# Performance work log

Measured on AMD Instinct MI355X. Metric: run time of the kernel, lower is better.

Reference implementation:

```python
import jax, jax.numpy as jnp
import numpy as np

B, S, L = 2, 1024, 1024
DIM_Q, H, K, D_C, D_CQ, R = 2048, 16, 128, 512, 1536, 64


def _rope_tables(length, dim):
    # matches _RoPECache._build_tables: repeat_interleave(2) layout
    inv = 1.0 / (10000.0 ** (jnp.arange(0, dim, 2, dtype=jnp.float32) / dim))
    f = jnp.arange(length, dtype=jnp.float32)[:, None] * inv[None, :]  # [len, dim/2]
    sin = jnp.repeat(jnp.sin(f), 2, axis=-1)
    cos = jnp.repeat(jnp.cos(f), 2, axis=-1)
    return sin, cos


def _rotate_half(x):
    half = x.shape[-1] // 2
    return jnp.concatenate([-x[..., half:], x[..., :half]], axis=-1)


def _apply_rope(x, sin, cos):
    return x * cos + _rotate_half(x) * sin


def setup_inputs() -> dict:
    key = jax.random.key(0)
    ks = jax.random.split(key, 8)
    return {
        "hidden_q": jax.random.normal(ks[0], (B, S, DIM_Q), jnp.float32),
        "kv_c": jax.random.normal(ks[1], (B, L, D_C), jnp.float32),
        "Wq": jax.random.normal(ks[2], (H * K, DIM_Q), jnp.float32) / np.sqrt(DIM_Q).astype(np.float32),
        "w_kc_q": jax.random.normal(ks[3], (H, K, D_CQ), jnp.float32) / np.sqrt(K).astype(np.float32),
        "w_kc_kv": jax.random.normal(ks[4], (H, K, D_C), jnp.float32) / np.sqrt(K).astype(np.float32),
        "W_qr": jax.random.normal(ks[5], (H, D_CQ, R), jnp.float32) / np.float32(np.sqrt(D_CQ) * np.sqrt(R)),
        "W_kr": jax.random.normal(ks[6], (H, D_C, R), jnp.float32) / np.sqrt(D_C).astype(np.float32),
        "Wo": jax.random.normal(ks[7], (DIM_Q, H * K), jnp.float32) / np.sqrt(H * K).astype(np.float32),
    }


def reference(hidden_q, kv_c, Wq, w_kc_q, w_kc_kv, W_qr, W_kr, Wo):
    Bv, Sv, _ = hidden_q.shape
    _, Lv, _ = kv_c.shape
    # latent -> per-head queries, then decompress to d_cq
    q_hk = (hidden_q @ Wq.T).reshape(Bv, Sv, H, K)          # [B,S,H,K]
    q_big = jnp.einsum('bshk,hkq->bshq', q_hk, w_kc_q)      # [B,S,H,d_cq]
    sin_q, cos_q = _rope_tables(Sv, D_CQ)
    q_big = _apply_rope(q_big, sin_q[None, :, None, :], cos_q[None, :, None, :])
    sin_k, cos_k = _rope_tables(Lv, D_C)
    kv_r = _apply_rope(kv_c, sin_k[None], cos_k[None])      # [B,L,d_c]
    # retrieval projections (scale 1/sqrt(r) baked into W_qr)
    q_r = jnp.einsum('bshq,hqr->bhsr', q_big, W_qr)         # [B,H,S,r]
    k_r = jnp.einsum('bld,hdr->bhlr', kv_r, W_kr)           # [B,H,L,r]
    scores = jnp.einsum('bhsr,bhlr->bhsl', q_r, k_r)
    attn = jax.nn.softmax(scores, axis=-1)
    # values are the (RoPE'd) compressed kv shared across heads
    ctx_c = jnp.einsum('bhsl,bld->bhsd', attn, kv_r)        # [B,H,S,d_c]
    # decompress context: w_kc_kv.transpose(1,2) is [H,d_c,K]
    ctx_lat = jnp.einsum('bhsd,hkd->bhsk', ctx_c, w_kc_kv)  # [B,H,S,K]
    ctx = ctx_lat.transpose(0, 2, 1, 3).reshape(Bv, Sv, H * K)
    return ctx @ Wo.T
```

## Files before the change

### kernel.cpp

```cpp
#include <hip/hip_runtime.h>
#include <hip/hip_bf16.h>


typedef __attribute__((ext_vector_type(8))) short short8;
typedef __attribute__((ext_vector_type(4))) float f32x4;

__device__ __forceinline__ unsigned short f2bs(float v){
  __hip_bfloat16 b = __float2bfloat16(v);
  return *reinterpret_cast<unsigned short*>(&b);
}
__device__ __forceinline__ void storeC(float* p, float v){ *p = v; }
__device__ __forceinline__ void storeC(unsigned short* p, float v){ *p = f2bs(v); }

__device__ __forceinline__ void gl_lds16(const void* g, void* l){
  __builtin_amdgcn_global_load_lds(
      (const __attribute__((address_space(1))) unsigned int*)g,
      (__attribute__((address_space(3))) unsigned int*)l, 16, 0, 0);
}

template<int N> __device__ __forceinline__ void wait_vmcnt(){
  if constexpr (N==0)       asm volatile("s_waitcnt vmcnt(0)" ::: "memory");
  else if constexpr (N==3)  asm volatile("s_waitcnt vmcnt(3)" ::: "memory");
  else if constexpr (N==4)  asm volatile("s_waitcnt vmcnt(4)" ::: "memory");
  else if constexpr (N==6)  asm volatile("s_waitcnt vmcnt(6)" ::: "memory");
  else if constexpr (N==8)  asm volatile("s_waitcnt vmcnt(8)" ::: "memory");
  else if constexpr (N==14) asm volatile("s_waitcnt vmcnt(14)" ::: "memory");
  else if constexpr (N==16) asm volatile("s_waitcnt vmcnt(16)" ::: "memory");
  else if constexpr (N==22) asm volatile("s_waitcnt vmcnt(22)" ::: "memory");
  else static_assert(N==0, "unsupported vmcnt");
}

__global__ __launch_bounds__(256) void prep_all(
    float4* __restrict__ rq,
    float* __restrict__ sink, float* __restrict__ cosk,
    const float* __restrict__ hidden, unsigned short* __restrict__ hiddenb,
    const float* __restrict__ Wq, unsigned short* __restrict__ Wqb,
    const float* __restrict__ wkckv, unsigned short* __restrict__ wkckvb,
    const float* __restrict__ Wo, unsigned short* __restrict__ Wob)
{
  int blk = blockIdx.x;
  if (blk < 3072){
    int idx = blk*256 + threadIdx.x;
    int s = idx / 768, j = idx - (idx/768)*768;
    int i1 = j >> 1;
    const float cst = -0.011992631f;
    float f1 = (float)s * __expf(cst * (float)i1);
    float f2 = (float)s * __expf(cst * (float)(384 + i1));
    float s1, c1, s2, c2;
    __sincosf(f1, &s1, &c1);
    __sincosf(f2, &s2, &c2);
    rq[idx] = make_float4(c1, s1, c2, s2);
    return;
  }
  if (blk < 4096){
    int idx = (blk-3072)*256 + threadIdx.x;
    int l = idx >> 8, j = idx & 255;
    const float cst = -0.035977892f;
    float f = (float)l * __expf(cst * (float)j);
    float sv, cv; __sincosf(f, &sv, &cv);
    int base = l*512 + 2*j;
    sink[base] = sv; sink[base+1] = sv;
    cosk[base] = cv; cosk[base+1] = cv;
    return;
  }
  const float* in; unsigned short* out; int i;
  if (blk < 8192){ in = hidden; out = hiddenb; i = (blk-4096)*256 + threadIdx.x; }
  else if (blk < 12288){ in = Wq; out = Wqb; i = (blk-8192)*256 + threadIdx.x; }
  else if (blk < 13312){ in = wkckv; out = wkckvb; i = (blk-12288)*256 + threadIdx.x; }
  else { in = Wo; out = Wob; i = (blk-13312)*256 + threadIdx.x; }
  float4 v = *(const float4*)(in + (long)i*4);
  ushort4 u; u.x=f2bs(v.x); u.y=f2bs(v.y); u.z=f2bs(v.z); u.w=f2bs(v.w);
  *(ushort4*)(out + (long)i*4) = u;
}

__global__ __launch_bounds__(256) void transpose_cvt(
    const float* __restrict__ in, unsigned short* __restrict__ out,
    int R, int Cn, long sIn, long sOut)
{
  __shared__ float tile[32][33];
  const float* ip = in + (long)blockIdx.z*sIn;
  unsigned short* op = out + (long)blockIdx.z*sOut;
  int c0 = blockIdx.x*32, r0 = blockIdx.y*32;
  int tr = threadIdx.x>>5, tc = threadIdx.x&31;
  #pragma unroll
  for (int i=0;i<4;i++)
    tile[tr+i*8][tc] = ip[(long)(r0+tr+i*8)*Cn + c0+tc];
  __syncthreads();
  #pragma unroll
  for (int i=0;i<4;i++)
    op[(long)(c0+tr+i*8)*R + r0+tc] = f2bs(tile[tc][tr+i*8]);
}

template<int BM,int BN,int WM,int WN,typename TC>
__global__ __launch_bounds__(256) void gemm_mfma(
    const unsigned short* __restrict__ A, const unsigned short* __restrict__ B,
    TC* __restrict__ C,
    int Kd, int lda, int ldb, int ldc, int Hb,
    long sAb, long sAh, long sBb, long sBh, long sCb, long sCh)
{
  constexpr int MF = WM/16, NF = WN/16;
  constexpr int WGM = BM/WM;
  constexpr int AOPS = (4*BM)/256;
  constexpr int BOPS = (4*BN)/256;
  constexpr int STG  = AOPS + BOPS;

  const int z = blockIdx.z, bb = z/Hb, hh = z - bb*Hb;
  const unsigned short* Ap = A + bb*sAb + hh*sAh;
  const unsigned short* Bp = B + bb*sBb + hh*sBh;
  TC* Cp = C + bb*sCb + hh*sCh;
  const int m0 = blockIdx.x*BM, n0 = blockIdx.y*BN;
  const int t = threadIdx.x, w = t>>6, l = t&63;
  const int wm0 = (w % WGM)*WM, wn0 = (w / WGM)*WN;
  const int lq = l>>4, lm = l&15;

  __shared__ __align__(16) unsigned short As[4][4*BM*8];
  __shared__ __align__(16) unsigned short Bs[4][4*BN*8];

  f32x4 acc[MF][NF];
  #pragma unroll
  for (int mf=0; mf<MF; ++mf)
    #pragma unroll
    for (int nf=0; nf<NF; ++nf)
      acc[mf][nf] = f32x4{0.f,0.f,0.f,0.f};

  auto stage = [&](int buf, int k0){
    #pragma unroll
    for (int o = 0; o < AOPS; ++o){
      int g = o*256 + t;
      int row = g & (BM-1), kq = g / BM;
      gl_lds16(Ap + (long)(m0+row)*lda + k0 + kq*8, &As[buf][(o*256 + w*64)*8]);
    }
    #pragma unroll
    for (int o = 0; o < BOPS; ++o){
      int g = o*256 + t;
      int row = g & (BN-1), kq = g / BN;
      gl_lds16(Bp + (long)(n0+row)*ldb + k0 + kq*8, &Bs[buf][(o*256 + w*64)*8]);
    }
  };

  const int nIter = Kd >> 5;
  stage(0, 0);
  if (1 < nIter) stage(1, 32);
  if (2 < nIter) stage(2, 64);

  for (int it = 0; it < nIter; ++it){
    const int cur = it & 3;
    const int rem = nIter - it;
    if (rem >= 3)      wait_vmcnt<2*STG>();
    else if (rem == 2) wait_vmcnt<STG>();
    else               wait_vmcnt<0>();
    __builtin_amdgcn_s_barrier();

    short8 af[MF], bfr[NF];
    #pragma unroll
    for (int mf=0; mf<MF; ++mf)
      af[mf] = *(const short8*)&As[cur][(lq*BM + wm0 + mf*16 + lm)*8];
    #pragma unroll
    for (int nf=0; nf<NF; ++nf)
      bfr[nf] = *(const short8*)&Bs[cur][(lq*BN + wn0 + nf*16 + lm)*8];
    #pragma unroll
    for (int mf=0; mf<MF; ++mf)
      #pragma unroll
      for (int nf=0; nf<NF; ++nf)
        acc[mf][nf] = __builtin_amdgcn_mfma_f32_16x16x32_bf16(
            af[mf], bfr[nf], acc[mf][nf], 0, 0, 0);

    if (it+3 < nIter) stage((it+3) & 3, (it+3)*32);
  }

  #pragma unroll
  for (int mf=0; mf<MF; ++mf){
    #pragma unroll
    for (int nf=0; nf<NF; ++nf){
      int row = m0 + wm0 + mf*16 + lq*4;
      int col = n0 + wn0 + nf*16 + lm;
      #pragma unroll
      for (int r=0; r<4; ++r)
        storeC(&Cp[(long)(row+r)*ldc + col], acc[mf][nf][r]);
    }
  }
}

__global__ __launch_bounds__(256) void q_fused(
    const unsigned short* __restrict__ A,
    const unsigned short* __restrict__ W1t,
    const unsigned short* __restrict__ W2t,
    const float4* __restrict__ rq,
    unsigned short* __restrict__ qrOut)
{
  const int z = blockIdx.z, bb = z>>4, hh = z&15;
  const int m0 = blockIdx.x*64;
  const unsigned short* Ap = A + (long)bb*2097152 + hh*128;
  const unsigned short* W1 = W1t + (long)hh*196608;
  const unsigned short* W2 = W2t + (long)hh*98304;
  unsigned short* qo = qrOut + ((long)z*1024 + m0)*64;

  const int t = threadIdx.x, w = t>>6, l = t&63;
  const int lq = l>>4, lm = l&15;

  __shared__ __align__(16) unsigned short As[16*64*8];
  __shared__ __align__(16) unsigned short W1s[2][16*64*8];
  __shared__ __align__(16) unsigned short W2s[2][8*64*8];
  __shared__ __align__(16) unsigned short Ps[64*72];

  #pragma unroll
  for (int o=0;o<4;++o){
    int g=o*256+t; int row=g&63, kq=g>>6;
    gl_lds16(Ap + (long)(m0+row)*2048 + kq*8, &As[(o*256+w*64)*8]);
  }
  auto stageW = [&](int buf, int cn){
    #pragma unroll
    for (int o=0;o<4;++o){
      int g=o*256+t; int row=g&63, kq=g>>6;
      int grow = (row<32) ? (cn*32+row) : (736+cn*32+row);
      gl_lds16(W1 + (long)grow*128 + kq*8, &W1s[buf][(o*256+w*64)*8]);
    }
    #pragma unroll
    for (int o=0;o<2;++o){
      int g=o*256+t; int n=g&63, kq=g>>6;
      int qk = (kq<4) ? (cn*32+kq*8) : (736+cn*32+kq*8);
      gl_lds16(W2 + (long)n*1536 + qk, &W2s[buf][(o*256+w*64)*8]);
    }
  };
  stageW(0, 0);
  __syncthreads();

  short8 af[4];
  #pragma unroll
  for (int ks=0; ks<4; ++ks)
    af[ks] = *(const short8*)&As[((ks*4+lq)*64 + w*16 + lm)*8];

  f32x4 accr[4];
  #pragma unroll
  for (int nf=0; nf<4; ++nf) accr[nf] = f32x4{0.f,0.f,0.f,0.f};

  for (int cn = 0; cn < 24; ++cn){
    const int cur = cn & 1;

    float4 rc_reg[2][4];
    #pragma unroll
    for (int nf=0; nf<2; ++nf)
      #pragma unroll
      for (int r=0; r<4; ++r){
        int srow = m0 + w*16 + lq*4 + r;
        rc_reg[nf][r] = rq[(long)srow*768 + cn*32 + nf*16 + lm];
      }
    if (cn < 23) stageW(cur^1, cn+1);
    if (cn < 23) wait_vmcnt<14>(); else wait_vmcnt<8>();
    __builtin_amdgcn_s_barrier();

    f32x4 sa[4];
    #pragma unroll
    for (int nf=0; nf<4; ++nf) sa[nf] = f32x4{0.f,0.f,0.f,0.f};
    #pragma unroll
    for (int ks=0; ks<4; ++ks)
      #pragma unroll
      for (int nf=0; nf<4; ++nf){
        short8 bf = *(const short8*)&W1s[cur][((ks*4+lq)*64 + nf*16 + lm)*8];
        sa[nf] = __builtin_amdgcn_mfma_f32_16x16x32_bf16(af[ks], bf, sa[nf], 0,0,0);
      }

    #pragma unroll
    for (int nf=0; nf<2; ++nf)
      #pragma unroll
      for (int r=0; r<4; ++r){
        int prow = w*16 + lq*4 + r;
        float4 rc = rc_reg[nf][r];
        float xl = sa[nf][r], xh = sa[nf+2][r];
        Ps[prow*72 + nf*16 + lm]      = f2bs(xl*rc.x - xh*rc.y);
        Ps[prow*72 + 32 + nf*16 + lm] = f2bs(xh*rc.z + xl*rc.w);
      }

    #pragma unroll
    for (int ks=0; ks<2; ++ks){
      short8 ap = *(const short8*)&Ps[(w*16 + lm)*72 + ks*32 + lq*8];
      #pragma unroll
      for (int nf=0; nf<4; ++nf){
        short8 bw = *(const short8*)&W2s[cur][((ks*4+lq)*64 + nf*16 + lm)*8];
        accr[nf] = __builtin_amdgcn_mfma_f32_16x16x32_bf16(ap, bw, accr[nf], 0,0,0);
      }
    }
    __builtin_amdgcn_s_barrier();
  }

  #pragma unroll
  for (int nf=0; nf<4; ++nf)
    #pragma unroll
    for (int r=0; r<4; ++r)
      qo[(long)(w*16 + lq*4 + r)*64 + nf*16 + lm] = f2bs(accr[nf][r]);
}

__global__ __launch_bounds__(256) void rope_k_kernel(
    const float* __restrict__ kc,
    const float* __restrict__ sk, const float* __restrict__ ck,
    unsigned short* __restrict__ kvrb)
{
  int idx = blockIdx.x*256 + threadIdx.x;
  int row = idx >> 8;
  int d = idx & 255;
  int l = row & 1023;
  long base = (long)row*512;
  float xl = kc[base+d], xh = kc[base+d+256];
  int tb = l*512 + d;
  kvrb[base+d]     = f2bs(xl*ck[tb]     - xh*sk[tb]);
  kvrb[base+d+256] = f2bs(xh*ck[tb+256] + xl*sk[tb+256]);
}

__global__ __launch_bounds__(256) void flash_mfma(
    const unsigned short* __restrict__ qr, const unsigned short* __restrict__ kr,
    const unsigned short* __restrict__ vt, unsigned short* __restrict__ ctx)
{
  const int b = blockIdx.z, h = blockIdx.y, s0 = blockIdx.x*64;
  const int t = threadIdx.x, w = t>>6, l = t&63;
  const int lq = l>>4, lm = l&15;

  __shared__ __align__(16) unsigned short Qs[8*64*8];
  __shared__ __align__(16) unsigned short Ks[2][8*64*8];
  __shared__ __align__(16) unsigned short Vts[2][8*128*8];
  __shared__ __align__(16) unsigned short Ps[64*72];

  const unsigned short* qbase = qr + ((long)(b*16+h)*1024 + s0)*64;
  const unsigned short* kbase = kr + (long)(b*16+h)*65536;
  const unsigned short* vbase = vt + (long)(b*16+h)*131072;

  auto stageKV = [&](int buf, int l0){
    #pragma unroll
    for (int o = 0; o < 2; ++o){
      int g = o*256 + t;
      int row = g & 63, kq = g >> 6;
      gl_lds16(kbase + (long)(l0+row)*64 + kq*8, &Ks[buf][(o*256 + w*64)*8]);
    }
    #pragma unroll
    for (int o = 0; o < 4; ++o){
      int g = o*256 + t;
      int row = g & 127, kq = g >> 7;
      gl_lds16(vbase + (long)row*1024 + l0 + kq*8, &Vts[buf][(o*256 + w*64)*8]);
    }
  };

  #pragma unroll
  for (int o = 0; o < 2; ++o){
    int g = o*256 + t;
    int row = g & 63, kq = g >> 6;
    gl_lds16(qbase + (long)row*64 + kq*8, &Qs[(o*256 + w*64)*8]);
  }
  stageKV(0, 0);
  __syncthreads();
  short8 aq[2];
  #pragma unroll
  for (int ks = 0; ks < 2; ++ks)
    aq[ks] = *(const short8*)&Qs[((ks*4+lq)*64 + w*16 + lm)*8];

  float m_run[4], l_run[4];
  #pragma unroll
  for (int r = 0; r < 4; ++r){ m_run[r] = -3e38f; l_run[r] = 0.f; }
  f32x4 acc_o[8];
  #pragma unroll
  for (int nf = 0; nf < 8; ++nf) acc_o[nf] = f32x4{0.f,0.f,0.f,0.f};

  for (int it = 0; it < 16; ++it){
    const int cur = it & 1;
    if (it < 15){ stageKV(cur^1, (it+1)*64); wait_vmcnt<6>(); }
    else        { wait_vmcnt<0>(); }
    __builtin_amdgcn_s_barrier();

    f32x4 acc_s[4];
    #pragma unroll
    for (int nf = 0; nf < 4; ++nf) acc_s[nf] = f32x4{0.f,0.f,0.f,0.f};
    #pragma unroll
    for (int ks = 0; ks < 2; ++ks)
      #pragma unroll
      for (int nf = 0; nf < 4; ++nf){
        short8 bf = *(const short8*)&Ks[cur][((ks*4+lq)*64 + nf*16 + lm)*8];
        acc_s[nf] = __builtin_amdgcn_mfma_f32_16x16x32_bf16(
            aq[ks], bf, acc_s[nf], 0, 0, 0);
      }

    float tmax[4];
    #pragma unroll
    for (int r = 0; r < 4; ++r)
      tmax[r] = fmaxf(fmaxf(acc_s[0][r], acc_s[1][r]),
                      fmaxf(acc_s[2][r], acc_s[3][r]));
    #pragma unroll
    for (int mask = 1; mask < 16; mask <<= 1)
      #pragma unroll
      for (int r = 0; r < 4; ++r)
        tmax[r] = fmaxf(tmax[r], __shfl_xor(tmax[r], mask));
    float alpha[4], rsum[4];
    #pragma unroll
    for (int r = 0; r < 4; ++r){
      float mnew = fmaxf(m_run[r], tmax[r]);
      alpha[r] = __expf(m_run[r] - mnew);
      m_run[r] = mnew;
      rsum[r] = 0.f;
    }
    #pragma unroll
    for (int nf = 0; nf < 4; ++nf)
      #pragma unroll
      for (int r = 0; r < 4; ++r){
        float p = __expf(acc_s[nf][r] - m_run[r]);
        rsum[r] += p;
        Ps[(w*16 + lq*4 + r)*72 + nf*16 + lm] = f2bs(p);
      }
    #pragma unroll
    for (int mask = 1; mask < 16; mask <<= 1)
      #pragma unroll
      for (int r = 0; r < 4; ++r)
        rsum[r] += __shfl_xor(rsum[r], mask);
    #pragma unroll
    for (int r = 0; r < 4; ++r)
      l_run[r] = l_run[r]*alpha[r] + rsum[r];

    #pragma unroll
    for (int nf = 0; nf < 8; ++nf)
      #pragma unroll
      for (int r = 0; r < 4; ++r)
        acc_o[nf][r] *= alpha[r];

    short8 ap[2];
    #pragma unroll
    for (int ks = 0; ks < 2; ++ks)
      ap[ks] = *(const short8*)&Ps[(w*16 + lm)*72 + ks*32 + lq*8];
    #pragma unroll
    for (int ks = 0; ks < 2; ++ks)
      #pragma unroll
      for (int nf = 0; nf < 8; ++nf){
        short8 bv = *(const short8*)&Vts[cur][((ks*4+lq)*128 + nf*16 + lm)*8];
        acc_o[nf] = __builtin_amdgcn_mfma_f32_16x16x32_bf16(
            ap[ks], bv, acc_o[nf], 0, 0, 0);
      }
    __builtin_amdgcn_s_barrier();
  }

  float inv[4];
  #pragma unroll
  for (int r = 0; r < 4; ++r) inv[r] = 1.f / l_run[r];
  #pragma unroll
  for (int nf = 0; nf < 8; ++nf)
    #pragma unroll
    for (int r = 0; r < 4; ++r){
      long row = (long)b*1024 + s0 + w*16 + lq*4 + r;
      ctx[row*2048 + h*128 + nf*16 + lm] = f2bs(acc_o[nf][r]*inv[r]);
    }
}

extern "C" void kernel_launch(void* const* d_in, const int* in_sizes, int n_in,
                              void* d_out, int out_size, void* d_ws, size_t ws_size,
                              hipStream_t stream)
{
  const float* hidden_q = (const float*)d_in[0];
  const float* kv_c     = (const float*)d_in[1];
  const float* Wq       = (const float*)d_in[2];
  const float* w_kc_q   = (const float*)d_in[3];
  const float* w_kc_kv  = (const float*)d_in[4];
  const float* W_qr     = (const float*)d_in[5];
  const float* W_kr     = (const float*)d_in[6];
  const float* Wo       = (const float*)d_in[7];
  float* out = (float*)d_out;

  char* wsb = (char*)d_ws;
  size_t off = 0;
  auto take = [&](size_t bytes)->void*{
    void* p = wsb + off; off += (bytes + 255) & ~(size_t)255; return p;
  };
  unsigned short* q_rb  = (unsigned short*)take(4194304);
  unsigned short* k_rb  = (unsigned short*)take(4194304);
  unsigned short* kv_rb = (unsigned short*)take(2097152);
  float* sink   = (float*)take(2097152);
  float* cosk   = (float*)take(2097152);
  float4* ropeq4 = (float4*)take(12582912);
  unsigned short* q_hk   = (unsigned short*)take(8388608);
  unsigned short* wkcqT  = (unsigned short*)take(6291456);
  unsigned short* WqrT   = (unsigned short*)take(3145728);
  unsigned short* wkckvb = (unsigned short*)take(2097152);
  unsigned short* WkrT   = (unsigned short*)take(1048576);
  unsigned short* Vt     = (unsigned short*)take(8388608);
  unsigned short* hiddenb = (unsigned short*)take(8388608);
  unsigned short* Wqb     = (unsigned short*)take(8388608);
  unsigned short* Wob     = (unsigned short*)take(8388608);
  unsigned short* ctx_lat = (unsigned short*)take(8388608);

  prep_all<<<17408, 256, 0, stream>>>(ropeq4, sink, cosk,
      hidden_q, hiddenb, Wq, Wqb, w_kc_kv, wkckvb, Wo, Wob);
  transpose_cvt<<<dim3(48,4,16), 256, 0, stream>>>(w_kc_q, wkcqT, 128, 1536, 196608, 196608);
  transpose_cvt<<<dim3(2,48,16), 256, 0, stream>>>(W_qr, WqrT, 1536, 64, 98304, 98304);
  transpose_cvt<<<dim3(2,16,16), 256, 0, stream>>>(W_kr, WkrT, 512, 64, 32768, 32768);

  gemm_mfma<128,128,64,64,unsigned short><<<dim3(16,16,1),256,0,stream>>>(
      hiddenb, Wqb, q_hk, 2048, 2048,2048,2048, 1, 0,0, 0,0, 0,0);

  q_fused<<<dim3(16,1,32),256,0,stream>>>(q_hk, wkcqT, WqrT, ropeq4, q_rb);

  rope_k_kernel<<<2048, 256, 0, stream>>>(kv_c, sink, cosk, kv_rb);

  gemm_mfma<128,64,64,32,unsigned short><<<dim3(8,1,32),256,0,stream>>>(
      kv_rb, WkrT, k_rb, 512, 512,512,64, 16,
      524288,0, 0,32768, 1048576,65536);

  gemm_mfma<128,128,64,64,unsigned short><<<dim3(1,8,32),256,0,stream>>>(
      wkckvb, kv_rb, Vt, 512, 512,512,1024, 16,
      0,65536, 524288,0, 2097152,131072);

  flash_mfma<<<dim3(16,16,2),256,0,stream>>>(q_rb, k_rb, Vt, ctx_lat);

  gemm_mfma<128,128,64,64,float><<<dim3(16,16,1),256,0,stream>>>(
      ctx_lat, Wob, out, 2048, 2048,2048,2048, 1, 0,0, 0,0, 0,0);
}
```

Measured before the change: 343.5 us.

## Fuse prep kernels, compute K rope inline, and retile q_fused warps

Merges the three transpose_cvt launches and the rope_k kernel into the single prep_all launch. The K-side RoPE now computes sin/cos on the fly and writes rotated bf16 kv directly, which drops the sin/cos tables and their global round trip. q_fused changes its warp layout to 2x2 (32 rows by half the columns per warp), loads A fragments straight from global instead of through LDS, and adds an extra barrier before reading Ps. The aims are fewer launches, less memory traffic and better B-fragment reuse, at the cost of an extra sync per chunk in q_fused.

```diff
diff --git a/kernel.cpp b/kernel.cpp
--- a/kernel.cpp
+++ b/kernel.cpp
@@ -30,13 +30,30 @@
   else static_assert(N==0, "unsupported vmcnt");
 }
 
+__device__ __forceinline__ void transpose_tile(
+    const float* ip, unsigned short* op, int R, int Cn, int c0, int r0)
+{
+  __shared__ float tile[32][33];
+  int tr = threadIdx.x>>5, tc = threadIdx.x&31;
+  #pragma unroll
+  for (int i=0;i<4;i++)
+    tile[tr+i*8][tc] = ip[(long)(r0+tr+i*8)*Cn + c0+tc];
+  __syncthreads();
+  #pragma unroll
+  for (int i=0;i<4;i++)
+    op[(long)(c0+tr+i*8)*R + r0+tc] = f2bs(tile[tc][tr+i*8]);
+}
+
 __global__ __launch_bounds__(256) void prep_all(
     float4* __restrict__ rq,
-    float* __restrict__ sink, float* __restrict__ cosk,
+    const float* __restrict__ kvc, unsigned short* __restrict__ kvrb,
     const float* __restrict__ hidden, unsigned short* __restrict__ hiddenb,
     const float* __restrict__ Wq, unsigned short* __restrict__ Wqb,
     const float* __restrict__ wkckv, unsigned short* __restrict__ wkckvb,
-    const float* __restrict__ Wo, unsigned short* __restrict__ Wob)
+    const float* __restrict__ Wo, unsigned short* __restrict__ Wob,
+    const float* __restrict__ wkcq, unsigned short* __restrict__ wkcqT,
+    const float* __restrict__ Wqr, unsigned short* __restrict__ WqrT,
+    const float* __restrict__ Wkr, unsigned short* __restrict__ WkrT)
 {
   int blk = blockIdx.x;
   if (blk < 3072){
@@ -54,41 +71,55 @@
   }
   if (blk < 4096){
     int idx = (blk-3072)*256 + threadIdx.x;
-    int l = idx >> 8, j = idx & 255;
+    int i1 = idx & 127;
+    int l  = (idx >> 7) & 1023;
+    int bb = idx >> 17;
     const float cst = -0.035977892f;
-    float f = (float)l * __expf(cst * (float)j);
-    float sv, cv; __sincosf(f, &sv, &cv);
-    int base = l*512 + 2*j;
-    sink[base] = sv; sink[base+1] = sv;
-    cosk[base] = cv; cosk[base+1] = cv;
+    float f1 = (float)l * __expf(cst * (float)i1);
+    float f2 = (float)l * __expf(cst * (float)(128 + i1));
+    float s1,c1,s2,c2; __sincosf(f1,&s1,&c1); __sincosf(f2,&s2,&c2);
+    long base = ((long)bb*1024 + l)*512;
+    float2 xlo = *(const float2*)&kvc[base + 2*i1];
+    float2 xhi = *(const float2*)&kvc[base + 2*i1 + 256];
+    unsigned int lo = (unsigned)f2bs(xlo.x*c1 - xhi.x*s1)
+                    | ((unsigned)f2bs(xlo.y*c1 - xhi.y*s1) << 16);
+    unsigned int hi = (unsigned)f2bs(xhi.x*c2 + xlo.x*s2)
+                    | ((unsigned)f2bs(xhi.y*c2 + xlo.y*s2) << 16);
+    *(unsigned int*)&kvrb[base + 2*i1]       = lo;
+    *(unsigned int*)&kvrb[base + 2*i1 + 256] = hi;
     return;
   }
-  const float* in; unsigned short* out; int i;
-  if (blk < 8192){ in = hidden; out = hiddenb; i = (blk-4096)*256 + threadIdx.x; }
-  else if (blk < 12288){ in = Wq; out = Wqb; i = (blk-8192)*256 + threadIdx.x; }
-  else if (blk < 13312){ in = wkckv; out = wkckvb; i = (blk-12288)*256 + threadIdx.x; }
-  else { in = Wo; out = Wob; i = (blk-13312)*256 + threadIdx.x; }
-  float4 v = *(const float4*)(in + (long)i*4);
-  ushort4 u; u.x=f2bs(v.x); u.y=f2bs(v.y); u.z=f2bs(v.z); u.w=f2bs(v.w);
-  *(ushort4*)(out + (long)i*4) = u;
-}
-
-__global__ __launch_bounds__(256) void transpose_cvt(
-    const float* __restrict__ in, unsigned short* __restrict__ out,
-    int R, int Cn, long sIn, long sOut)
-{
-  __shared__ float tile[32][33];
-  const float* ip = in + (long)blockIdx.z*sIn;
-  unsigned short* op = out + (long)blockIdx.z*sOut;
-  int c0 = blockIdx.x*32, r0 = blockIdx.y*32;
-  int tr = threadIdx.x>>5, tc = threadIdx.x&31;
-  #pragma unroll
-  for (int i=0;i<4;i++)
-    tile[tr+i*8][tc] = ip[(long)(r0+tr+i*8)*Cn + c0+tc];
-  __syncthreads();
-  #pragma unroll
-  for (int i=0;i<4;i++)
-    op[(long)(c0+tr+i*8)*R + r0+tc] = f2bs(tile[tc][tr+i*8]);
+  if (blk < 17408){
+    const float* in; unsigned short* out; int i;
+    if (blk < 8192){ in = hidden; out = hiddenb; i = (blk-4096)*256 + threadIdx.x; }
+    else if (blk < 12288){ in = Wq; out = Wqb; i = (blk-8192)*256 + threadIdx.x; }
+    else if (blk < 13312){ in = wkckv; out = wkckvb; i = (blk-12288)*256 + threadIdx.x; }
+    else { in = Wo; out = Wob; i = (blk-13312)*256 + threadIdx.x; }
+    float4 v = *(const float4*)(in + (long)i*4);
+    ushort4 u; u.x=f2bs(v.x); u.y=f2bs(v.y); u.z=f2bs(v.z); u.w=f2bs(v.w);
+    *(ushort4*)(out + (long)i*4) = u;
+    return;
+  }
+  if (blk < 20480){
+    int b2 = blk - 17408;
+    int x = b2 % 48, rem = b2 / 48, y = rem % 4, z = rem >> 2;
+    transpose_tile(wkcq + (long)z*196608, wkcqT + (long)z*196608,
+                   128, 1536, x*32, y*32);
+    return;
+  }
+  if (blk < 22016){
+    int b2 = blk - 20480;
+    int x = b2 & 1, rem = b2 >> 1, y = rem % 48, z = rem / 48;
+    transpose_tile(Wqr + (long)z*98304, WqrT + (long)z*98304,
+                   1536, 64, x*32, y*32);
+    return;
+  }
+  {
+    int b2 = blk - 22016;
+    int x = b2 & 1, y = (b2 >> 1) & 15, z = b2 >> 5;
+    transpose_tile(Wkr + (long)z*32768, WkrT + (long)z*32768,
+                   512, 64, x*32, y*32);
+  }
 }
 
 template<int BM,int BN,int WM,int WN,typename TC>
@@ -197,17 +228,20 @@
 
   const int t = threadIdx.x, w = t>>6, l = t&63;
   const int lq = l>>4, lm = l&15;
-
-  __shared__ __align__(16) unsigned short As[16*64*8];
+  const int wr = (w>>1)*32;
+  const int wc = w&1;
+
   __shared__ __align__(16) unsigned short W1s[2][16*64*8];
   __shared__ __align__(16) unsigned short W2s[2][8*64*8];
   __shared__ __align__(16) unsigned short Ps[64*72];
 
-  #pragma unroll
-  for (int o=0;o<4;++o){
-    int g=o*256+t; int row=g&63, kq=g>>6;
-    gl_lds16(Ap + (long)(m0+row)*2048 + kq*8, &As[(o*256+w*64)*8]);
-  }
+  short8 af[2][4];
+  #pragma unroll
+  for (int mf=0; mf<2; ++mf)
+    #pragma unroll
+    for (int ks=0; ks<4; ++ks)
+      af[mf][ks] = *(const short8*)&Ap[(long)(m0 + wr + mf*16 + lm)*2048 + (ks*4+lq)*8];
+
   auto stageW = [&](int buf, int cn){
     #pragma unroll
     for (int o=0;o<4;++o){
@@ -223,87 +257,78 @@
     }
   };
   stageW(0, 0);
-  __syncthreads();
-
-  short8 af[4];
-  #pragma unroll
-  for (int ks=0; ks<4; ++ks)
-    af[ks] = *(const short8*)&As[((ks*4+lq)*64 + w*16 + lm)*8];
-
-  f32x4 accr[4];
-  #pragma unroll
-  for (int nf=0; nf<4; ++nf) accr[nf] = f32x4{0.f,0.f,0.f,0.f};
+
+  f32x4 accr[2][2];
+  #pragma unroll
+  for (int mf=0; mf<2; ++mf)
+    #pragma unroll
+    for (int nf=0; nf<2; ++nf) accr[mf][nf] = f32x4{0.f,0.f,0.f,0.f};
 
   for (int cn = 0; cn < 24; ++cn){
     const int cur = cn & 1;
 
     float4 rc_reg[2][4];
     #pragma unroll
-    for (int nf=0; nf<2; ++nf)
+    for (int mf=0; mf<2; ++mf)
       #pragma unroll
       for (int r=0; r<4; ++r){
-        int srow = m0 + w*16 + lq*4 + r;
-        rc_reg[nf][r] = rq[(long)srow*768 + cn*32 + nf*16 + lm];
+        int srow = m0 + wr + mf*16 + lq*4 + r;
+        rc_reg[mf][r] = rq[(long)srow*768 + cn*32 + wc*16 + lm];
       }
     if (cn < 23) stageW(cur^1, cn+1);
     if (cn < 23) wait_vmcnt<14>(); else wait_vmcnt<8>();
     __builtin_amdgcn_s_barrier();
 
-    f32x4 sa[4];
-    #pragma unroll
-    for (int nf=0; nf<4; ++nf) sa[nf] = f32x4{0.f,0.f,0.f,0.f};
-    #pragma unroll
-    for (int ks=0; ks<4; ++ks)
-      #pragma unroll
-      for (int nf=0; nf<4; ++nf){
-        short8 bf = *(const short8*)&W1s[cur][((ks*4+lq)*64 + nf*16 + lm)*8];
-        sa[nf] = __builtin_amdgcn_mfma_f32_16x16x32_bf16(af[ks], bf, sa[nf], 0,0,0);
+    f32x4 sa[2][2];
+    #pragma unroll
+    for (int mf=0; mf<2; ++mf)
+      #pragma unroll
+      for (int p=0; p<2; ++p) sa[mf][p] = f32x4{0.f,0.f,0.f,0.f};
+    #pragma unroll
+    for (int ks=0; ks<4; ++ks){
+      short8 blo = *(const short8*)&W1s[cur][((ks*4+lq)*64 + wc*16 + lm)*8];
+      short8 bhi = *(const short8*)&W1s[cur][((ks*4+lq)*64 + 32 + wc*16 + lm)*8];
+      sa[0][0] = __builtin_amdgcn_mfma_f32_16x16x32_bf16(af[0][ks], blo, sa[0][0], 0,0,0);
+      sa[0][1] = __builtin_amdgcn_mfma_f32_16x16x32_bf16(af[0][ks], bhi, sa[0][1], 0,0,0);
+      sa[1][0] = __builtin_amdgcn_mfma_f32_16x16x32_bf16(af[1][ks], blo, sa[1][0], 0,0,0);
+      sa[1][1] = __builtin_amdgcn_mfma_f32_16x16x32_bf16(af[1][ks], bhi, sa[1][1], 0,0,0);
+    }
+
+    #pragma unroll
+    for (int mf=0; mf<2; ++mf)
+      #pragma unroll
+      for (int r=0; r<4; ++r){
+        int prow = wr + mf*16 + lq*4 + r;
+        float4 rc = rc_reg[mf][r];
+        float xl = sa[mf][0][r], xh = sa[mf][1][r];
+        Ps[prow*72 + wc*16 + lm]      = f2bs(xl*rc.x - xh*rc.y);
+        Ps[prow*72 + 32 + wc*16 + lm] = f2bs(xh*rc.z + xl*rc.w);
       }
-
+    asm volatile("s_waitcnt lgkmcnt(0)" ::: "memory");
+    __builtin_amdgcn_sched_barrier(0);
+    __builtin_amdgcn_s_barrier();
+
+    #pragma unroll
+    for (int ks=0; ks<2; ++ks){
+      short8 ap0 = *(const short8*)&Ps[(wr + lm)*72 + ks*32 + lq*8];
+      short8 ap1 = *(const short8*)&Ps[(wr + 16 + lm)*72 + ks*32 + lq*8];
+      #pragma unroll
+      for (int nf=0; nf<2; ++nf){
+        short8 bw = *(const short8*)&W2s[cur][((ks*4+lq)*64 + wc*32 + nf*16 + lm)*8];
+        accr[0][nf] = __builtin_amdgcn_mfma_f32_16x16x32_bf16(ap0, bw, accr[0][nf], 0,0,0);
+        accr[1][nf] = __builtin_amdgcn_mfma_f32_16x16x32_bf16(ap1, bw, accr[1][nf], 0,0,0);
+      }
+    }
+    __builtin_amdgcn_s_barrier();
+  }
+
+  #pragma unroll
+  for (int mf=0; mf<2; ++mf)
     #pragma unroll
     for (int nf=0; nf<2; ++nf)
       #pragma unroll
-      for (int r=0; r<4; ++r){
-        int prow = w*16 + lq*4 + r;
-        float4 rc = rc_reg[nf][r];
-        float xl = sa[nf][r], xh = sa[nf+2][r];
-        Ps[prow*72 + nf*16 + lm]      = f2bs(xl*rc.x - xh*rc.y);
-        Ps[prow*72 + 32 + nf*16 + lm] = f2bs(xh*rc.z + xl*rc.w);
-      }
-
-    #pragma unroll
-    for (int ks=0; ks<2; ++ks){
-      short8 ap = *(const short8*)&Ps[(w*16 + lm)*72 + ks*32 + lq*8];
-      #pragma unroll
-      for (int nf=0; nf<4; ++nf){
-        short8 bw = *(const short8*)&W2s[cur][((ks*4+lq)*64 + nf*16 + lm)*8];
-        accr[nf] = __builtin_amdgcn_mfma_f32_16x16x32_bf16(ap, bw, accr[nf], 0,0,0);
-      }
-    }
-    __builtin_amdgcn_s_barrier();
-  }
-
-  #pragma unroll
-  for (int nf=0; nf<4; ++nf)
-    #pragma unroll
-    for (int r=0; r<4; ++r)
-      qo[(long)(w*16 + lq*4 + r)*64 + nf*16 + lm] = f2bs(accr[nf][r]);
-}
-
-__global__ __launch_bounds__(256) void rope_k_kernel(
-    const float* __restrict__ kc,
-    const float* __restrict__ sk, const float* __restrict__ ck,
-    unsigned short* __restrict__ kvrb)
-{
-  int idx = blockIdx.x*256 + threadIdx.x;
-  int row = idx >> 8;
-  int d = idx & 255;
-  int l = row & 1023;
-  long base = (long)row*512;
-  float xl = kc[base+d], xh = kc[base+d+256];
-  int tb = l*512 + d;
-  kvrb[base+d]     = f2bs(xl*ck[tb]     - xh*sk[tb]);
-  kvrb[base+d+256] = f2bs(xh*ck[tb+256] + xl*sk[tb+256]);
+      for (int r=0; r<4; ++r)
+        qo[(long)(wr + mf*16 + lq*4 + r)*64 + wc*32 + nf*16 + lm] = f2bs(accr[mf][nf][r]);
 }
 
 __global__ __launch_bounds__(256) void flash_mfma(
@@ -466,8 +491,6 @@
   unsigned short* q_rb  = (unsigned short*)take(4194304);
   unsigned short* k_rb  = (unsigned short*)take(4194304);
   unsigned short* kv_rb = (unsigned short*)take(2097152);
-  float* sink   = (float*)take(2097152);
-  float* cosk   = (float*)take(2097152);
   float4* ropeq4 = (float4*)take(12582912);
   unsigned short* q_hk   = (unsigned short*)take(8388608);
   unsigned short* wkcqT  = (unsigned short*)take(6291456);
@@ -480,18 +503,15 @@
   unsigned short* Wob     = (unsigned short*)take(8388608);
   unsigned short* ctx_lat = (unsigned short*)take(8388608);
 
-  prep_all<<<17408, 256, 0, stream>>>(ropeq4, sink, cosk,
-      hidden_q, hiddenb, Wq, Wqb, w_kc_kv, wkckvb, Wo, Wob);
-  transpose_cvt<<<dim3(48,4,16), 256, 0, stream>>>(w_kc_q, wkcqT, 128, 1536, 196608, 196608);
-  transpose_cvt<<<dim3(2,48,16), 256, 0, stream>>>(W_qr, WqrT, 1536, 64, 98304, 98304);
-  transpose_cvt<<<dim3(2,16,16), 256, 0, stream>>>(W_kr, WkrT, 512, 64, 32768, 32768);
+  prep_all<<<22528, 256, 0, stream>>>(ropeq4,
+      kv_c, kv_rb,
+      hidden_q, hiddenb, Wq, Wqb, w_kc_kv, wkckvb, Wo, Wob,
+      w_kc_q, wkcqT, W_qr, WqrT, W_kr, WkrT);
 
   gemm_mfma<128,128,64,64,unsigned short><<<dim3(16,16,1),256,0,stream>>>(
       hiddenb, Wqb, q_hk, 2048, 2048,2048,2048, 1, 0,0, 0,0, 0,0);
 
   q_fused<<<dim3(16,1,32),256,0,stream>>>(q_hk, wkcqT, WqrT, ropeq4, q_rb);
-
-  rope_k_kernel<<<2048, 256, 0, stream>>>(kv_c, sink, cosk, kv_rb);
 
   gemm_mfma<128,64,64,32,unsigned short><<<dim3(8,1,32),256,0,stream>>>(
       kv_rb, WkrT, k_rb, 512, 512,512,64, 16,
```

Result: faster. 333.6 us (-2.9%).
